# Kernel optimization log

Hardware: AMD Instinct MI355X
Metric: run time of the kernel (lower is better)

The kernel has to match this reference:

```python
import jax, jax.numpy as jnp
import numpy as np

B, N, DIM = 2, 2048, 1024
NUM_HEADS = 16
EFF = NUM_HEADS // 2          # 8 effective heads
HD = DIM // NUM_HEADS         # 64
LAMBDA_INIT = 0.8
EPS = 1e-5


def setup_inputs() -> dict:
    key = jax.random.key(0)
    ks = jax.random.split(key, 16)
    s = 0.02
    return {
        "x":  jax.random.normal(ks[0], (B, N, DIM), dtype=jnp.float32),
        "Wq": jax.random.normal(ks[1], (DIM, DIM), dtype=jnp.float32) * s,
        "bq": jnp.zeros((DIM,), dtype=jnp.float32),
        "Wk": jax.random.normal(ks[2], (DIM, DIM), dtype=jnp.float32) * s,
        "bk": jnp.zeros((DIM,), dtype=jnp.float32),
        "Wv": jax.random.normal(ks[3], (DIM, DIM), dtype=jnp.float32) * s,
        "bv": jnp.zeros((DIM,), dtype=jnp.float32),
        "Wo": jax.random.normal(ks[4], (DIM, DIM), dtype=jnp.float32) * s,
        "bo": jnp.zeros((DIM,), dtype=jnp.float32),
        "norm_w": jnp.ones((2 * HD,), dtype=jnp.float32),
        "lq1": jax.random.normal(ks[5], (HD,), dtype=jnp.float32) * 0.1,
        "lk1": jax.random.normal(ks[6], (HD,), dtype=jnp.float32) * 0.1,
        "lq2": jax.random.normal(ks[7], (HD,), dtype=jnp.float32) * 0.1,
        "lk2": jax.random.normal(ks[8], (HD,), dtype=jnp.float32) * 0.1,
    }


def reference(x, Wq, bq, Wk, bk, Wv, bv, Wo, bo, norm_w, lq1, lk1, lq2, lk2):
    scale = HD ** -0.5
    # projections (torch Linear: y = x @ W.T + b)
    q = (x @ Wq.T + bq).reshape(B, N, NUM_HEADS, HD).transpose(0, 2, 1, 3) * scale  # [B,2E,N,hd]
    k = (x @ Wk.T + bk).reshape(B, N, NUM_HEADS, HD).transpose(0, 2, 1, 3)          # [B,2E,N,hd]
    v = (x @ Wv.T + bv).reshape(B, N, EFF, 2 * HD).transpose(0, 2, 1, 3)            # [B,E,N,2hd]

    scores = jnp.einsum('bhqd,bhkd->bhqk', q, k)              # [B,2E,N,N]
    probs = jax.nn.softmax(scores, axis=-1)
    probs = probs.reshape(B, EFF, 2, N, N)                    # pair consecutive heads

    lam = jnp.exp(jnp.sum(lq1 * lk1)) - jnp.exp(jnp.sum(lq2 * lk2)) + LAMBDA_INIT
    diff = probs[:, :, 0] - lam * probs[:, :, 1]              # [B,E,N,N]

    out = jnp.einsum('behk,bekd->behd'.replace('e','h').replace('hh','h') if False else 'bhqk,bhkd->bhqd', diff, v)  # [B,E,N,2hd]
    # headwise RMSNorm over last dim (2*hd)
    out = out * jax.lax.rsqrt(jnp.mean(out * out, axis=-1, keepdims=True) + EPS) * norm_w
    out = out * (1.0 - LAMBDA_INIT)

    out = out.transpose(0, 2, 1, 3).reshape(B, N, DIM)
    return out @ Wo.T + bo
```

## Files before the change

### kernel.cpp

```cpp
#include <hip/hip_runtime.h>
#include <hip/hip_bf16.h>

#define B_   2
#define N_   2048
#define DIM_ 1024
#define HD_  64
#define DV_  128

typedef __bf16 bf16;
typedef __bf16 bf16x8 __attribute__((ext_vector_type(8)));
typedef __bf16 bf16x4 __attribute__((ext_vector_type(4)));
typedef float  floatx4 __attribute__((ext_vector_type(4)));
typedef float  floatx16 __attribute__((ext_vector_type(16)));
typedef unsigned int uint;
typedef uint uint2v __attribute__((ext_vector_type(2)));
typedef uint uint4v __attribute__((ext_vector_type(4)));

#if __has_builtin(__builtin_amdgcn_exp2f)
#define EXP2(x) __builtin_amdgcn_exp2f(x)
#else
#define EXP2(x) exp2f(x)
#endif

#define QSCALE 0.1803368801111244f

__device__ __forceinline__ void async16(const void* g, void* l) {
  __builtin_amdgcn_global_load_lds(
      (__attribute__((address_space(1))) void*)g,
      (__attribute__((address_space(3))) void*)l, 16, 0, 0);
}

__device__ __forceinline__ uint packbf(float a, float b) {
  unsigned short ul = __builtin_bit_cast(unsigned short, (bf16)a);
  unsigned short uh = __builtin_bit_cast(unsigned short, (bf16)b);
  return (uint)ul | ((uint)uh << 16);
}

__global__ void convert_kernel(const float* __restrict__ x,
                               const float* __restrict__ wq,
                               const float* __restrict__ wk,
                               const float* __restrict__ wv,
                               const float* __restrict__ wo,
                               bf16* __restrict__ dst) {
  const int NX = B_ * N_ * DIM_;
  const int NW = DIM_ * DIM_;
  int i = (blockIdx.x * 256 + threadIdx.x) * 4;
  const float* src;
  int off;
  if (i < NX) { src = x; off = i; }
  else {
    int j = i - NX;
    int w = j >> 20;
    off = j & (NW - 1);
    src = (w == 0) ? wq : (w == 1) ? wk : (w == 2) ? wv : wo;
  }
  float4 v = *(const float4*)(src + off);
  bf16x4 o = { (bf16)v.x, (bf16)v.y, (bf16)v.z, (bf16)v.w };
  *(bf16x4*)(dst + i) = o;
}

__global__ void lam_kernel(const float* __restrict__ lq1, const float* __restrict__ lk1,
                           const float* __restrict__ lq2, const float* __restrict__ lk2,
                           float* __restrict__ lam_out) {
  int l = threadIdx.x;
  float a = lq1[l] * lk1[l];
  float b = lq2[l] * lk2[l];
  for (int m = 1; m < 64; m <<= 1) {
    a += __shfl_xor(a, m, 64);
    b += __shfl_xor(b, m, 64);
  }
  if (l == 0) *lam_out = __expf(a) - __expf(b) + 0.8f;
}

__global__ __launch_bounds__(256) void proj_kernel(
    const bf16* __restrict__ xb, const bf16* __restrict__ wall,
    const float* __restrict__ bq, const float* __restrict__ bk,
    const float* __restrict__ bv,
    bf16* __restrict__ qo, bf16* __restrict__ ko, bf16* __restrict__ vt) {
  __shared__ __align__(16) bf16 SM[2 * 128 * 64];
  bf16* At = SM;
  bf16* Bt = SM + 128 * 64;
  const int tid = threadIdx.x, lane = tid & 63, w = tid >> 6;
  const int tm = blockIdx.x, tn = blockIdx.y, z = blockIdx.z;
  const int quad = lane >> 4, l15 = lane & 15;
  const int wm = (w >> 1) * 64, wn = (w & 1) * 64;
  const bf16* Ab = xb + (long)tm * 128 * DIM_;
  const bf16* Bb = wall + (long)z * (DIM_ * DIM_) + (long)tn * 128 * DIM_;
  floatx4 zero = {0.f, 0.f, 0.f, 0.f};
  floatx4 acc[4][4];
#pragma unroll
  for (int i = 0; i < 4; ++i)
#pragma unroll
    for (int j = 0; j < 4; ++j) acc[i][j] = zero;

  for (int kb = 0; kb < DIM_ / 64; ++kb) {
    for (int idx = tid; idx < 1024; idx += 256) {
      int row = idx >> 3, ch = idx & 7, g = ch ^ (row & 7);
      async16(Ab + row * DIM_ + kb * 64 + g * 8, (char*)At + (idx - lane) * 16);
      async16(Bb + row * DIM_ + kb * 64 + g * 8, (char*)Bt + (idx - lane) * 16);
    }
    __syncthreads();
#pragma unroll
    for (int ks = 0; ks < 2; ++ks) {
      bf16x8 af[4], bfm[4];
#pragma unroll
      for (int mt = 0; mt < 4; ++mt) {
        int r = wm + mt * 16 + l15;
        af[mt] = *(const bf16x8*)&At[r * 64 + ((ks * 4 + quad) ^ (r & 7)) * 8];
      }
#pragma unroll
      for (int nt = 0; nt < 4; ++nt) {
        int r = wn + nt * 16 + l15;
        bfm[nt] = *(const bf16x8*)&Bt[r * 64 + ((ks * 4 + quad) ^ (r & 7)) * 8];
      }
#pragma unroll
      for (int mt = 0; mt < 4; ++mt)
#pragma unroll
        for (int nt = 0; nt < 4; ++nt)
          acc[mt][nt] = __builtin_amdgcn_mfma_f32_16x16x32_bf16(
              af[mt], bfm[nt], acc[mt][nt], 0, 0, 0);
    }
    __syncthreads();
  }

  if (z != 2) {
#pragma unroll
    for (int mt = 0; mt < 4; ++mt)
#pragma unroll
      for (int nt = 0; nt < 4; ++nt)
#pragma unroll
        for (int r = 0; r < 4; ++r) {
          int grow = tm * 128 + wm + mt * 16 + quad * 4 + r;
          int gcol = tn * 128 + wn + nt * 16 + l15;
          float v = acc[mt][nt][r];
          if (z == 0) {
            qo[(long)grow * DIM_ + gcol] = (bf16)((v + bq[gcol]) * QSCALE);
          } else {
            ko[(long)grow * DIM_ + gcol] = (bf16)(v + bk[gcol]);
          }
        }
  } else {
    bf16* Vl = SM;
#pragma unroll
    for (int nt = 0; nt < 4; ++nt) {
      int d = wn + nt * 16 + l15;
      float bvv = bv[tn * 128 + d];
      int m = (d & 7) * 2;
#pragma unroll
      for (int mt = 0; mt < 4; ++mt) {
        bf16x4 v4 = { (bf16)(acc[mt][nt][0] + bvv), (bf16)(acc[mt][nt][1] + bvv),
                      (bf16)(acc[mt][nt][2] + bvv), (bf16)(acc[mt][nt][3] + bvv) };
        int c = (wm >> 2) + mt * 4 + quad;
        *(bf16x4*)&Vl[d * 128 + (c ^ m) * 4] = v4;
      }
    }
    __syncthreads();
    const int bb = tm >> 4, e = tn;
    const long rowbase = ((long)(bb * 8 + e) * 128) * (long)N_ + (tm & 15) * 128;
#pragma unroll
    for (int p = 0; p < 8; ++p) {
      int d = p * 16 + (tid >> 4), j = tid & 15;
      int cs = (2 * j) ^ ((d & 7) * 2);
      bf16x8 val = *(const bf16x8*)&Vl[d * 128 + cs * 4];
      *(bf16x8*)&vt[rowbase + (long)d * N_ + j * 8] = val;
    }
  }
}

__global__ __launch_bounds__(512, 2) void attn_kernel(
    const bf16* __restrict__ qb, const bf16* __restrict__ kbuf,
    const bf16* __restrict__ vt, const float* __restrict__ lamp,
    const float* __restrict__ norm_w, bf16* __restrict__ ao) {
  __shared__ __align__(16) char smem[65536];

  const int tid = threadIdx.x, lane = tid & 63, w = tid >> 6;
  const int qt = blockIdx.x, e = blockIdx.y, b = blockIdx.z;
  const int hl = w & 1, qh = w >> 1;
  const int h = lane >> 5, l31 = lane & 31;
  const int qbase = qt * 128;

  bf16x8 qf[4];
  {
    const bf16* qrp = qb + (long)(b * N_ + qbase + qh * 32 + l31) * DIM_
                      + e * 128 + hl * 64 + h * 8;
#pragma unroll
    for (int c = 0; c < 4; ++c) qf[c] = *(const bf16x8*)(qrp + c * 16);
  }

  const bf16* kbase = kbuf + (long)b * N_ * DIM_ + e * 128;
  const bf16* vbase = vt + (long)(b * 8 + e) * DV_ * N_;

  floatx16 acc[4];
#pragma unroll
  for (int dt = 0; dt < 4; ++dt) acc[dt] = floatx16{};
  float lp = 0.f;

#define STAGE(ktv, bufv)                                                            \
  {                                                                                 \
    int kt_ = (ktv);                                                                \
    char* kdst = smem + (bufv) * 16384;                                             \
    char* vdst = smem + 32768 + (bufv) * 16384;                                     \
    _Pragma("unroll") for (int t = 0; t < 2; ++t) {                                 \
      int idx = tid + t * 512;                                                      \
      int khl = idx >> 9, row = (idx >> 3) & 63, ch = idx & 7;                      \
      int g = ch ^ (row & 7) ^ ((row >> 3) & 3);                                    \
      async16(kbase + ((long)(kt_ * 64 + row)) * DIM_ + khl * 64 + g * 8,           \
              kdst + (idx - lane) * 16);                                            \
    }                                                                               \
    _Pragma("unroll") for (int t = 0; t < 2; ++t) {                                 \
      int idx = tid + t * 512;                                                      \
      int row = idx >> 3, ch = idx & 7;                                             \
      int g = ch ^ (row & 7) ^ ((row >> 3) & 3);                                    \
      async16(vbase + (long)row * N_ + kt_ * 64 + g * 8,                            \
              vdst + (idx - lane) * 16);                                            \
    }                                                                               \
  }

  STAGE(0, 0);

  for (int kt = 0; kt < N_ / 64; ++kt) {
    const int buf = kt & 1;
    __syncthreads();
    if (kt + 1 < N_ / 64) STAGE(kt + 1, buf ^ 1);

    const bf16* Kh = (const bf16*)(smem + buf * 16384) + hl * 4096;
    const bf16* Vb = (const bf16*)(smem + 32768 + buf * 16384);

    bf16x8 kfrag[2][4], vfrag[4][4];
#pragma unroll
    for (int kt2 = 0; kt2 < 2; ++kt2)
#pragma unroll
      for (int c = 0; c < 4; ++c) {
        int row = kt2 * 32 + l31;
        int sw = (c * 2 + h) ^ (row & 7) ^ ((row >> 3) & 3);
        kfrag[kt2][c] = *(const bf16x8*)&Kh[row * 64 + sw * 8];
      }
#pragma unroll
    for (int dt = 0; dt < 4; ++dt)
#pragma unroll
      for (int kc = 0; kc < 4; ++kc) {
        int row = dt * 32 + l31;
        int sw = (kc * 2 + h) ^ (row & 7) ^ ((row >> 3) & 3);
        vfrag[dt][kc] = *(const bf16x8*)&Vb[row * 64 + sw * 8];
      }

    bf16x8 af[2][2];
#pragma unroll
    for (int kt2 = 0; kt2 < 2; ++kt2) {
      floatx16 sv{};
#pragma unroll
      for (int c = 0; c < 4; ++c)
        sv = __builtin_amdgcn_mfma_f32_32x32x16_bf16(kfrag[kt2][c], qf[c], sv, 0, 0, 0);
      float t[16];
      float s = 0.f;
#pragma unroll
      for (int i = 0; i < 16; ++i) { t[i] = EXP2(sv[i]); s += t[i]; }
      lp += s;
      uint d0 = packbf(t[0], t[1]),   d1 = packbf(t[2], t[3]);
      uint d2 = packbf(t[4], t[5]),   d3 = packbf(t[6], t[7]);
      uint d4 = packbf(t[8], t[9]),   d5 = packbf(t[10], t[11]);
      uint d6 = packbf(t[12], t[13]), d7 = packbf(t[14], t[15]);
      uint4v f0, f1;
#if __has_builtin(__builtin_amdgcn_permlane32_swap)
      uint2v r02 = __builtin_amdgcn_permlane32_swap(d0, d2, false, false);
      uint2v r13 = __builtin_amdgcn_permlane32_swap(d1, d3, false, false);
      f0 = uint4v{r02.x, r13.x, r02.y, r13.y};
      uint2v r46 = __builtin_amdgcn_permlane32_swap(d4, d6, false, false);
      uint2v r57 = __builtin_amdgcn_permlane32_swap(d5, d7, false, false);
      f1 = uint4v{r46.x, r57.x, r46.y, r57.y};
#else
      uint e0 = __shfl_xor((int)d0, 32, 64), e1 = __shfl_xor((int)d1, 32, 64);
      uint e2 = __shfl_xor((int)d2, 32, 64), e3 = __shfl_xor((int)d3, 32, 64);
      uint e4 = __shfl_xor((int)d4, 32, 64), e5 = __shfl_xor((int)d5, 32, 64);
      uint e6 = __shfl_xor((int)d6, 32, 64), e7 = __shfl_xor((int)d7, 32, 64);
      f0 = h ? uint4v{e2, e3, d2, d3} : uint4v{d0, d1, e0, e1};
      f1 = h ? uint4v{e6, e7, d6, d7} : uint4v{d4, d5, e4, e5};
#endif
      af[kt2][0] = __builtin_bit_cast(bf16x8, f0);
      af[kt2][1] = __builtin_bit_cast(bf16x8, f1);
    }
#pragma unroll
    for (int dt = 0; dt < 4; ++dt)
#pragma unroll
      for (int kt2 = 0; kt2 < 2; ++kt2)
#pragma unroll
        for (int u = 0; u < 2; ++u)
          acc[dt] = __builtin_amdgcn_mfma_f32_32x32x16_bf16(
              af[kt2][u], vfrag[dt][kt2 * 2 + u], acc[dt], 0, 0, 0);
  }

  lp += __shfl_xor(lp, 32, 64);

  float* Ob = (float*)smem;
  __syncthreads();

  if (hl == 1) {
#pragma unroll
    for (int r = 0; r < 16; ++r) {
      int qloc = (r & 3) + 8 * (r >> 2) + 4 * h;
      float inv = 1.0f / __shfl(lp, qloc, 64);
      float* row = &Ob[(qh * 32 + qloc) * 128 + l31];
#pragma unroll
      for (int dt = 0; dt < 4; ++dt) row[dt * 32] = acc[dt][r] * inv;
    }
  }
  __syncthreads();
  if (hl == 0) {
    float lam = *lamp;
    float nw4[4];
#pragma unroll
    for (int dt = 0; dt < 4; ++dt) nw4[dt] = norm_w[dt * 32 + l31] * 0.2f;
#pragma unroll
    for (int r = 0; r < 16; ++r) {
      int qloc = (r & 3) + 8 * (r >> 2) + 4 * h;
      float inv = 1.0f / __shfl(lp, qloc, 64);
      const float* row = &Ob[(qh * 32 + qloc) * 128 + l31];
      float v[4], ss = 0.f;
#pragma unroll
      for (int dt = 0; dt < 4; ++dt) {
        v[dt] = acc[dt][r] * inv - lam * row[dt * 32];
        ss += v[dt] * v[dt];
      }
#pragma unroll
      for (int msk = 1; msk < 32; msk <<= 1) ss += __shfl_xor(ss, msk, 64);
      float rms = rsqrtf(ss * (1.0f / 128.0f) + 1e-5f);
      int n = qbase + qh * 32 + qloc;
      bf16* dst = ao + (long)(b * N_ + n) * DIM_ + e * DV_ + l31;
#pragma unroll
      for (int dt = 0; dt < 4; ++dt) dst[dt * 32] = (bf16)(v[dt] * rms * nw4[dt]);
    }
  }
}

__global__ __launch_bounds__(512) void out_gemm(
    const bf16* __restrict__ ab, const bf16* __restrict__ wo,
    const float* __restrict__ bo, float* __restrict__ out) {
  __shared__ __align__(16) bf16 At[128 * 64];
  __shared__ __align__(16) bf16 Bt[128 * 64];
  const int tid = threadIdx.x, lane = tid & 63, w = tid >> 6;
  const int tm = blockIdx.x, tn = blockIdx.y;
  const int quad = lane >> 4, l15 = lane & 15;
  const int wm = (w & 3) * 32, wn = (w >> 2) * 64;
  const bf16* Ab = ab + (long)tm * 128 * DIM_;
  const bf16* Bb = wo + (long)tn * 128 * DIM_;
  floatx4 zero = {0.f, 0.f, 0.f, 0.f};
  floatx4 acc[2][4];
#pragma unroll
  for (int i = 0; i < 2; ++i)
#pragma unroll
    for (int j = 0; j < 4; ++j) acc[i][j] = zero;

  for (int kb = 0; kb < DIM_ / 64; ++kb) {
    for (int idx = tid; idx < 1024; idx += 512) {
      int row = idx >> 3, ch = idx & 7, g = ch ^ (row & 7);
      async16(Ab + row * DIM_ + kb * 64 + g * 8, (char*)At + (idx - lane) * 16);
      async16(Bb + row * DIM_ + kb * 64 + g * 8, (char*)Bt + (idx - lane) * 16);
    }
    __syncthreads();
#pragma unroll
    for (int ks = 0; ks < 2; ++ks) {
      bf16x8 af[2], bfm[4];
#pragma unroll
      for (int mt = 0; mt < 2; ++mt) {
        int r = wm + mt * 16 + l15;
        af[mt] = *(const bf16x8*)&At[r * 64 + ((ks * 4 + quad) ^ (r & 7)) * 8];
      }
#pragma unroll
      for (int nt = 0; nt < 4; ++nt) {
        int r = wn + nt * 16 + l15;
        bfm[nt] = *(const bf16x8*)&Bt[r * 64 + ((ks * 4 + quad) ^ (r & 7)) * 8];
      }
#pragma unroll
      for (int mt = 0; mt < 2; ++mt)
#pragma unroll
        for (int nt = 0; nt < 4; ++nt)
          acc[mt][nt] = __builtin_amdgcn_mfma_f32_16x16x32_bf16(
              af[mt], bfm[nt], acc[mt][nt], 0, 0, 0);
    }
    __syncthreads();
  }
#pragma unroll
  for (int mt = 0; mt < 2; ++mt)
#pragma unroll
    for (int nt = 0; nt < 4; ++nt)
#pragma unroll
      for (int r = 0; r < 4; ++r) {
        int grow = tm * 128 + wm + mt * 16 + quad * 4 + r;
        int gcol = tn * 128 + wn + nt * 16 + l15;
        out[(long)grow * DIM_ + gcol] = acc[mt][nt][r] + bo[gcol];
      }
}

extern "C" void kernel_launch(void* const* d_in, const int* in_sizes, int n_in,
                              void* d_out, int out_size, void* d_ws, size_t ws_size,
                              hipStream_t stream) {
  const float* x    = (const float*)d_in[0];
  const float* Wq   = (const float*)d_in[1];
  const float* bq   = (const float*)d_in[2];
  const float* Wk   = (const float*)d_in[3];
  const float* bk   = (const float*)d_in[4];
  const float* Wv   = (const float*)d_in[5];
  const float* bv   = (const float*)d_in[6];
  const float* Wo   = (const float*)d_in[7];
  const float* bo   = (const float*)d_in[8];
  const float* nw   = (const float*)d_in[9];
  const float* lq1  = (const float*)d_in[10];
  const float* lk1  = (const float*)d_in[11];
  const float* lq2  = (const float*)d_in[12];
  const float* lk2  = (const float*)d_in[13];

  char* ws = (char*)d_ws;
  float* lam = (float*)ws;
  bf16* xb   = (bf16*)(ws + 256);
  bf16* wqb  = xb + 4194304;
  bf16* qb   = wqb + 4 * 1048576;
  bf16* kbuf = qb + 4194304;
  bf16* vtb  = kbuf + 4194304;
  bf16* ab   = vtb + 4194304;

  convert_kernel<<<8192, 256, 0, stream>>>(x, Wq, Wk, Wv, Wo, xb);
  lam_kernel<<<1, 64, 0, stream>>>(lq1, lk1, lq2, lk2, lam);
  proj_kernel<<<dim3(32, 8, 3), 256, 0, stream>>>(xb, wqb, bq, bk, bv, qb, kbuf, vtb);
  attn_kernel<<<dim3(16, 8, 2), 512, 0, stream>>>(qb, kbuf, vtb, lam, nw, ab);
  out_gemm<<<dim3(32, 8), 512, 0, stream>>>(ab, wqb + 3 * 1048576, bo, (float*)d_out);
}
```

Baseline: 212.5 us.

## Split attention key tiles across two wave groups with 1024-thread blocks

Doubles the attention block to 1024 threads. Each half of the waves handles one 32-key half of every 64-key tile, so per-wave work and register pressure per iteration are halved. Partial row sums and output accumulators from the two halves are combined through shared memory before the differential-lambda subtraction and RMSNorm. This raises the number of waves in flight on the 256-block grid, at the cost of a larger shared-memory footprint, extra reduction passes and barriers, and a launch_bounds(1024,4) request that may not be achievable.

```diff
diff --git a/kernel.cpp b/kernel.cpp
--- a/kernel.cpp
+++ b/kernel.cpp
@@ -167,15 +167,16 @@
   }
 }
 
-__global__ __launch_bounds__(512, 2) void attn_kernel(
+__global__ __launch_bounds__(1024, 4) void attn_kernel(
     const bf16* __restrict__ qb, const bf16* __restrict__ kbuf,
     const bf16* __restrict__ vt, const float* __restrict__ lamp,
     const float* __restrict__ norm_w, bf16* __restrict__ ao) {
-  __shared__ __align__(16) char smem[65536];
+  __shared__ __align__(16) char smem[131072];
+  __shared__ float Ls[512];
 
   const int tid = threadIdx.x, lane = tid & 63, w = tid >> 6;
   const int qt = blockIdx.x, e = blockIdx.y, b = blockIdx.z;
-  const int hl = w & 1, qh = w >> 1;
+  const int hl = w & 1, qh = (w >> 1) & 3, cp = w >> 3;
   const int h = lane >> 5, l31 = lane & 31;
   const int qbase = qt * 128;
 
@@ -200,15 +201,15 @@
     int kt_ = (ktv);                                                                \
     char* kdst = smem + (bufv) * 16384;                                             \
     char* vdst = smem + 32768 + (bufv) * 16384;                                     \
-    _Pragma("unroll") for (int t = 0; t < 2; ++t) {                                 \
-      int idx = tid + t * 512;                                                      \
+    {                                                                               \
+      int idx = tid;                                                                \
       int khl = idx >> 9, row = (idx >> 3) & 63, ch = idx & 7;                      \
       int g = ch ^ (row & 7) ^ ((row >> 3) & 3);                                    \
       async16(kbase + ((long)(kt_ * 64 + row)) * DIM_ + khl * 64 + g * 8,           \
               kdst + (idx - lane) * 16);                                            \
     }                                                                               \
-    _Pragma("unroll") for (int t = 0; t < 2; ++t) {                                 \
-      int idx = tid + t * 512;                                                      \
+    {                                                                               \
+      int idx = tid;                                                                \
       int row = idx >> 3, ch = idx & 7;                                             \
       int g = ch ^ (row & 7) ^ ((row >> 3) & 3);                                    \
       async16(vbase + (long)row * N_ + kt_ * 64 + g * 8,                            \
@@ -226,86 +227,112 @@
     const bf16* Kh = (const bf16*)(smem + buf * 16384) + hl * 4096;
     const bf16* Vb = (const bf16*)(smem + 32768 + buf * 16384);
 
-    bf16x8 kfrag[2][4], vfrag[4][4];
-#pragma unroll
-    for (int kt2 = 0; kt2 < 2; ++kt2)
-#pragma unroll
-      for (int c = 0; c < 4; ++c) {
-        int row = kt2 * 32 + l31;
-        int sw = (c * 2 + h) ^ (row & 7) ^ ((row >> 3) & 3);
-        kfrag[kt2][c] = *(const bf16x8*)&Kh[row * 64 + sw * 8];
-      }
+    bf16x8 kfrag[4], vfrag[4][2];
+#pragma unroll
+    for (int c = 0; c < 4; ++c) {
+      int row = cp * 32 + l31;
+      int sw = (c * 2 + h) ^ (row & 7) ^ ((row >> 3) & 3);
+      kfrag[c] = *(const bf16x8*)&Kh[row * 64 + sw * 8];
+    }
 #pragma unroll
     for (int dt = 0; dt < 4; ++dt)
 #pragma unroll
-      for (int kc = 0; kc < 4; ++kc) {
+      for (int u = 0; u < 2; ++u) {
+        int kc = cp * 2 + u;
         int row = dt * 32 + l31;
         int sw = (kc * 2 + h) ^ (row & 7) ^ ((row >> 3) & 3);
-        vfrag[dt][kc] = *(const bf16x8*)&Vb[row * 64 + sw * 8];
-      }
-
-    bf16x8 af[2][2];
-#pragma unroll
-    for (int kt2 = 0; kt2 < 2; ++kt2) {
-      floatx16 sv{};
-#pragma unroll
-      for (int c = 0; c < 4; ++c)
-        sv = __builtin_amdgcn_mfma_f32_32x32x16_bf16(kfrag[kt2][c], qf[c], sv, 0, 0, 0);
-      float t[16];
-      float s = 0.f;
-#pragma unroll
-      for (int i = 0; i < 16; ++i) { t[i] = EXP2(sv[i]); s += t[i]; }
-      lp += s;
-      uint d0 = packbf(t[0], t[1]),   d1 = packbf(t[2], t[3]);
-      uint d2 = packbf(t[4], t[5]),   d3 = packbf(t[6], t[7]);
-      uint d4 = packbf(t[8], t[9]),   d5 = packbf(t[10], t[11]);
-      uint d6 = packbf(t[12], t[13]), d7 = packbf(t[14], t[15]);
-      uint4v f0, f1;
+        vfrag[dt][u] = *(const bf16x8*)&Vb[row * 64 + sw * 8];
+      }
+
+    floatx16 sv{};
+#pragma unroll
+    for (int c = 0; c < 4; ++c)
+      sv = __builtin_amdgcn_mfma_f32_32x32x16_bf16(kfrag[c], qf[c], sv, 0, 0, 0);
+    float t[16];
+    float s = 0.f;
+#pragma unroll
+    for (int i = 0; i < 16; ++i) { t[i] = EXP2(sv[i]); s += t[i]; }
+    lp += s;
+    uint d0 = packbf(t[0], t[1]),   d1 = packbf(t[2], t[3]);
+    uint d2 = packbf(t[4], t[5]),   d3 = packbf(t[6], t[7]);
+    uint d4 = packbf(t[8], t[9]),   d5 = packbf(t[10], t[11]);
+    uint d6 = packbf(t[12], t[13]), d7 = packbf(t[14], t[15]);
+    uint4v f0, f1;
 #if __has_builtin(__builtin_amdgcn_permlane32_swap)
-      uint2v r02 = __builtin_amdgcn_permlane32_swap(d0, d2, false, false);
-      uint2v r13 = __builtin_amdgcn_permlane32_swap(d1, d3, false, false);
-      f0 = uint4v{r02.x, r13.x, r02.y, r13.y};
-      uint2v r46 = __builtin_amdgcn_permlane32_swap(d4, d6, false, false);
-      uint2v r57 = __builtin_amdgcn_permlane32_swap(d5, d7, false, false);
-      f1 = uint4v{r46.x, r57.x, r46.y, r57.y};
+    uint2v r02 = __builtin_amdgcn_permlane32_swap(d0, d2, false, false);
+    uint2v r13 = __builtin_amdgcn_permlane32_swap(d1, d3, false, false);
+    f0 = uint4v{r02.x, r13.x, r02.y, r13.y};
+    uint2v r46 = __builtin_amdgcn_permlane32_swap(d4, d6, false, false);
+    uint2v r57 = __builtin_amdgcn_permlane32_swap(d5, d7, false, false);
+    f1 = uint4v{r46.x, r57.x, r46.y, r57.y};
 #else
-      uint e0 = __shfl_xor((int)d0, 32, 64), e1 = __shfl_xor((int)d1, 32, 64);
-      uint e2 = __shfl_xor((int)d2, 32, 64), e3 = __shfl_xor((int)d3, 32, 64);
-      uint e4 = __shfl_xor((int)d4, 32, 64), e5 = __shfl_xor((int)d5, 32, 64);
-      uint e6 = __shfl_xor((int)d6, 32, 64), e7 = __shfl_xor((int)d7, 32, 64);
-      f0 = h ? uint4v{e2, e3, d2, d3} : uint4v{d0, d1, e0, e1};
-      f1 = h ? uint4v{e6, e7, d6, d7} : uint4v{d4, d5, e4, e5};
+    uint e0 = __shfl_xor((int)d0, 32, 64), e1 = __shfl_xor((int)d1, 32, 64);
+    uint e2 = __shfl_xor((int)d2, 32, 64), e3 = __shfl_xor((int)d3, 32, 64);
+    uint e4 = __shfl_xor((int)d4, 32, 64), e5 = __shfl_xor((int)d5, 32, 64);
+    uint e6 = __shfl_xor((int)d6, 32, 64), e7 = __shfl_xor((int)d7, 32, 64);
+    f0 = h ? uint4v{e2, e3, d2, d3} : uint4v{d0, d1, e0, e1};
+    f1 = h ? uint4v{e6, e7, d6, d7} : uint4v{d4, d5, e4, e5};
 #endif
-      af[kt2][0] = __builtin_bit_cast(bf16x8, f0);
-      af[kt2][1] = __builtin_bit_cast(bf16x8, f1);
-    }
-#pragma unroll
-    for (int dt = 0; dt < 4; ++dt)
-#pragma unroll
-      for (int kt2 = 0; kt2 < 2; ++kt2)
-#pragma unroll
-        for (int u = 0; u < 2; ++u)
-          acc[dt] = __builtin_amdgcn_mfma_f32_32x32x16_bf16(
-              af[kt2][u], vfrag[dt][kt2 * 2 + u], acc[dt], 0, 0, 0);
+    bf16x8 af0 = __builtin_bit_cast(bf16x8, f0);
+    bf16x8 af1 = __builtin_bit_cast(bf16x8, f1);
+#pragma unroll
+    for (int dt = 0; dt < 4; ++dt) {
+      acc[dt] = __builtin_amdgcn_mfma_f32_32x32x16_bf16(af0, vfrag[dt][0], acc[dt], 0, 0, 0);
+      acc[dt] = __builtin_amdgcn_mfma_f32_32x32x16_bf16(af1, vfrag[dt][1], acc[dt], 0, 0, 0);
+    }
   }
 
   lp += __shfl_xor(lp, 32, 64);
-
-  float* Ob = (float*)smem;
+  if (h == 0) Ls[cp * 256 + hl * 128 + qh * 32 + l31] = lp;
   __syncthreads();
-
-  if (hl == 1) {
+  float lptot = Ls[hl * 128 + qh * 32 + l31] + Ls[256 + hl * 128 + qh * 32 + l31];
+
+  float* S = (float*)smem;
+  float* T = (float*)(smem + 65536);
+
+  if (hl == 1 && cp == 0) {
 #pragma unroll
     for (int r = 0; r < 16; ++r) {
       int qloc = (r & 3) + 8 * (r >> 2) + 4 * h;
-      float inv = 1.0f / __shfl(lp, qloc, 64);
-      float* row = &Ob[(qh * 32 + qloc) * 128 + l31];
+      float inv = 1.0f / __shfl(lptot, qloc, 64);
+      float* row = &S[(qh * 32 + qloc) * 128 + l31];
 #pragma unroll
       for (int dt = 0; dt < 4; ++dt) row[dt * 32] = acc[dt][r] * inv;
     }
   }
+  if (hl == 0 && cp == 1) {
+#pragma unroll
+    for (int r = 0; r < 16; ++r) {
+      int qloc = (r & 3) + 8 * (r >> 2) + 4 * h;
+      float inv = 1.0f / __shfl(lptot, qloc, 64);
+      float* row = &T[(qh * 32 + qloc) * 128 + l31];
+#pragma unroll
+      for (int dt = 0; dt < 4; ++dt) row[dt * 32] = acc[dt][r] * inv;
+    }
+  }
   __syncthreads();
-  if (hl == 0) {
+  if (hl == 1 && cp == 1) {
+#pragma unroll
+    for (int r = 0; r < 16; ++r) {
+      int qloc = (r & 3) + 8 * (r >> 2) + 4 * h;
+      float inv = 1.0f / __shfl(lptot, qloc, 64);
+      float* row = &S[(qh * 32 + qloc) * 128 + l31];
+#pragma unroll
+      for (int dt = 0; dt < 4; ++dt) row[dt * 32] += acc[dt][r] * inv;
+    }
+  }
+  if (hl == 0 && cp == 0) {
+#pragma unroll
+    for (int r = 0; r < 16; ++r) {
+      int qloc = (r & 3) + 8 * (r >> 2) + 4 * h;
+      float inv = 1.0f / __shfl(lptot, qloc, 64);
+      const float* row = &T[(qh * 32 + qloc) * 128 + l31];
+#pragma unroll
+      for (int dt = 0; dt < 4; ++dt) acc[dt][r] = acc[dt][r] * inv + row[dt * 32];
+    }
+  }
+  __syncthreads();
+  if (hl == 0 && cp == 0) {
     float lam = *lamp;
     float nw4[4];
 #pragma unroll
@@ -313,12 +340,11 @@
 #pragma unroll
     for (int r = 0; r < 16; ++r) {
       int qloc = (r & 3) + 8 * (r >> 2) + 4 * h;
-      float inv = 1.0f / __shfl(lp, qloc, 64);
-      const float* row = &Ob[(qh * 32 + qloc) * 128 + l31];
+      const float* row = &S[(qh * 32 + qloc) * 128 + l31];
       float v[4], ss = 0.f;
 #pragma unroll
       for (int dt = 0; dt < 4; ++dt) {
-        v[dt] = acc[dt][r] * inv - lam * row[dt * 32];
+        v[dt] = acc[dt][r] - lam * row[dt * 32];
         ss += v[dt] * v[dt];
       }
 #pragma unroll
@@ -421,6 +447,6 @@
   convert_kernel<<<8192, 256, 0, stream>>>(x, Wq, Wk, Wv, Wo, xb);
   lam_kernel<<<1, 64, 0, stream>>>(lq1, lk1, lq2, lk2, lam);
   proj_kernel<<<dim3(32, 8, 3), 256, 0, stream>>>(xb, wqb, bq, bk, bv, qb, kbuf, vtb);
-  attn_kernel<<<dim3(16, 8, 2), 512, 0, stream>>>(qb, kbuf, vtb, lam, nw, ab);
+  attn_kernel<<<dim3(16, 8, 2), 1024, 0, stream>>>(qb, kbuf, vtb, lam, nw, ab);
   out_gemm<<<dim3(32, 8), 512, 0, stream>>>(ab, wqb + 3 * 1048576, bo, (float*)d_out);
 }
```

Measured after the change: 217.7 us. 1.02x slower.
